# Optimization experiments

Hardware: AMD Instinct MI355X
Metric: run time of the kernel (lower is better)

Reference implementation:

```python
import jax, jax.numpy as jnp
import numpy as np

B, D, H, E = 4096, 256, 1024, 8


def setup_inputs() -> dict:
    key = jax.random.key(0)
    k_x, k_w1, k_b1, k_w2, k_b2, k_idx = jax.random.split(key, 6)
    return {
        "x": jax.random.normal(k_x, (B, D), dtype=jnp.float32),
        "W1": jax.random.normal(k_w1, (E, D, H), dtype=jnp.float32) * (1.0 / np.sqrt(D)),
        "b1": jax.random.normal(k_b1, (E, H), dtype=jnp.float32) * 0.01,
        "W2": jax.random.normal(k_w2, (E, H, D), dtype=jnp.float32) * (1.0 / np.sqrt(H)),
        "b2": jax.random.normal(k_b2, (E, D), dtype=jnp.float32) * 0.01,
        "expert_idx": jax.random.randint(k_idx, (B,), 0, E, dtype=jnp.int64)
        if jax.config.jax_enable_x64 else jax.random.randint(k_idx, (B,), 0, E, dtype=jnp.int32),
    }


def reference(x, W1, b1, W2, b2, expert_idx):
    # Each sample i is routed to expert expert_idx[i] (= video_id_to_index lookup),
    # runs the expert MLP on its batch-of-1 row, and results are concatenated.
    # Vectorized as: run all experts over the batch, combine with a one-hot mask.
    E_ = W1.shape[0]
    onehot = jax.nn.one_hot(expert_idx, E_, dtype=x.dtype)          # [B, E]
    h = jax.nn.relu(jnp.einsum("bd,edh->ebh", x, W1) + b1[:, None, :])  # [E, B, H]
    y = jnp.einsum("ebh,ehd->ebd", h, W2) + b2[:, None, :]              # [E, B, D]
    return jnp.einsum("be,ebd->bd", onehot, y)                           # [B, D]
```

## Files before the change

kernel.cpp:

```cpp
#include <hip/hip_runtime.h>


#define D_DIM 256
#define H_DIM 1024
#define E_NUM 8
#define B_TOK 4096
#define CAP   1024

typedef __attribute__((ext_vector_type(8))) short short8;
typedef __attribute__((ext_vector_type(4))) float f32x4;
typedef unsigned short u16;
typedef unsigned int u32;
typedef unsigned long long u64;

#define CNT_OFF    0
#define BUCKET_OFF 1024
#define XB_OFF     (BUCKET_OFF + E_NUM*B_TOK*4)
#define W1T_OFF    (XB_OFF  + (size_t)B_TOK*D_DIM*2)
#define W2T_OFF    (W1T_OFF + (size_t)E_NUM*H_DIM*D_DIM*2)
#define HW_OFF     (W2T_OFF + (size_t)E_NUM*D_DIM*H_DIM*2)

__device__ __forceinline__ u16 f2bf(float f) {
    u32 u = __builtin_bit_cast(u32, f);
    u = (u + 0x7fffu + ((u >> 16) & 1u)) >> 16;
    return (u16)u;
}

__device__ __forceinline__ void trans_load(const float* __restrict__ in, int C,
                                           int rt, int ct, int tt, u16* tile) {
    #pragma unroll
    for (int it = 0; it < 4; ++it) {
        int r = it * 16 + (tt >> 4);
        int c4 = (tt & 15) * 4;
        float4 v = *(const float4*)(in + (size_t)(rt * 64 + r) * C + ct * 64 + c4);
        u64 pk = (u64)f2bf(v.x) | ((u64)f2bf(v.y) << 16)
               | ((u64)f2bf(v.z) << 32) | ((u64)f2bf(v.w) << 48);
        *(u64*)&tile[r * 68 + c4] = pk;
    }
}

__device__ __forceinline__ uint4 trans_pack(const u16* tile, int oc, int r0) {
    u32 p0 = tile[(r0 + 0) * 68 + oc] | ((u32)tile[(r0 + 1) * 68 + oc] << 16);
    u32 p1 = tile[(r0 + 2) * 68 + oc] | ((u32)tile[(r0 + 3) * 68 + oc] << 16);
    u32 p2 = tile[(r0 + 4) * 68 + oc] | ((u32)tile[(r0 + 5) * 68 + oc] << 16);
    u32 p3 = tile[(r0 + 6) * 68 + oc] | ((u32)tile[(r0 + 7) * 68 + oc] << 16);
    return uint4{p0, p1, p2, p3};
}

__global__ __launch_bounds__(256) void prep_kernel(
    const float* __restrict__ x, const float* __restrict__ W1,
    const float* __restrict__ W2, const int* __restrict__ eidx,
    int* __restrict__ cnt, int* __restrict__ bucket,
    u16* __restrict__ xb, u16* __restrict__ w1t, u16* __restrict__ w2t)
{
    __shared__ u16 tile[64 * 68];
    const int b = blockIdx.x, tid = threadIdx.x;
    if (b < 8) {
        __shared__ int wsum[4];
        const int e = b;
        const int lane = tid & 63, wv = tid >> 6;
        int base = 0;
        #pragma unroll
        for (int c = 0; c < 16; ++c) {
            int t = c * 256 + tid;
            bool m = (eidx[t] == e);
            u64 bal = __ballot(m);
            int pfx = __popcll(bal & ((1ull << lane) - 1ull));
            if (lane == 0) wsum[wv] = __popcll(bal);
            __syncthreads();
            int wb = 0, total = 0;
            #pragma unroll
            for (int i = 0; i < 4; ++i) { if (i < wv) wb += wsum[i]; total += wsum[i]; }
            if (m) bucket[e * B_TOK + base + wb + pfx] = t;
            base += total;
            __syncthreads();
        }
        if (tid == 0) cnt[e] = base;
    } else if (b < 264) {
        int gb = b - 8;
        int row = gb * 16 + (tid >> 4);
        int sub = tid & 15;
        const float* src = x + (size_t)row * D_DIM + sub * 16;
        u16* dst = xb + (size_t)row * D_DIM + sub * 16;
        #pragma unroll
        for (int i = 0; i < 4; ++i) {
            float4 v = *(const float4*)(src + i * 4);
            u64 pk = (u64)f2bf(v.x) | ((u64)f2bf(v.y) << 16)
                   | ((u64)f2bf(v.z) << 32) | ((u64)f2bf(v.w) << 48);
            *(u64*)(dst + i * 4) = pk;
        }
    } else if (b < 776) {
        int bb = b - 264;
        int e = bb >> 6, tj = bb & 63;
        int rt = tj >> 4, ct = tj & 15;
        trans_load(W1 + (size_t)e * D_DIM * H_DIM, H_DIM, rt, ct, tid, tile);
        __syncthreads();
        u16* outp = w1t + (size_t)e * H_DIM * D_DIM;
        #pragma unroll
        for (int it = 0; it < 2; ++it) {
            int oc = it * 32 + (tid >> 3);
            int r0 = (tid & 7) * 8;
            *(uint4*)(outp + (size_t)(ct * 64 + oc) * D_DIM + rt * 64 + r0) =
                trans_pack(tile, oc, r0);
        }
    } else {
        int bb = b - 776;
        int e = bb >> 6, tj = bb & 63;
        int rt = tj >> 2, ct = tj & 3;
        trans_load(W2 + (size_t)e * H_DIM * D_DIM, D_DIM, rt, ct, tid, tile);
        __syncthreads();
        u16* outp = w2t + (size_t)e * D_DIM * H_DIM;
        #pragma unroll
        for (int it = 0; it < 2; ++it) {
            int oc = it * 32 + (tid >> 3);
            int r0 = (tid & 7) * 8;
            *(uint4*)(outp + (size_t)(ct * 64 + oc) * H_DIM + rt * 64 + r0) =
                trans_pack(tile, oc, r0);
        }
    }
}

__global__ __launch_bounds__(256, 2) void gemm1_kernel(
    const u16* __restrict__ xb, const u16* __restrict__ w1t,
    const float* __restrict__ b1, const int* __restrict__ cnt,
    const int* __restrict__ bucket, u16* __restrict__ hw)
{
    __shared__ u16 xs[64 * 264];
    __shared__ u16 w1s[64 * 264];
    __shared__ u16 hs[64 * 72];

    const int b = blockIdx.x;
    const int e = b >> 8, tile = (b >> 4) & 15, hch = b & 15;
    const int n = min(cnt[e], CAP);
    const int row0 = tile * 64;
    if (row0 >= n) return;

    const int tid = threadIdx.x;
    const int w = tid >> 6, L = tid & 63, l15 = L & 15, l4 = L >> 4;
    const int wr = (w >> 1) * 32, wc = (w & 1) * 32;

    {
        const int rr = tid >> 5, cc = (tid & 31) * 8;
        int tok[8];
        #pragma unroll
        for (int it = 0; it < 8; ++it) {
            int grow = row0 + it * 8 + rr;
            tok[it] = grow < n ? bucket[e * B_TOK + grow] : 0;
        }
        const u16* gw = w1t + ((size_t)e * H_DIM + hch * 64) * D_DIM;
        #pragma unroll
        for (int it = 0; it < 8; ++it) {
            int row = it * 8 + rr;
            *(short8*)&xs[row * 264 + cc]  = *(const short8*)&xb[(size_t)tok[it] * D_DIM + cc];
            *(short8*)&w1s[row * 264 + cc] = *(const short8*)&gw[(size_t)row * D_DIM + cc];
        }
    }
    __syncthreads();

    f32x4 acc[2][2];
    #pragma unroll
    for (int i = 0; i < 2; ++i)
        #pragma unroll
        for (int j = 0; j < 2; ++j) acc[i][j] = (f32x4){0.f, 0.f, 0.f, 0.f};

    #pragma unroll
    for (int k = 0; k < 8; ++k) {
        short8 a0 = *(const short8*)&xs[(wr + l15) * 264 + k * 32 + l4 * 8];
        short8 a1 = *(const short8*)&xs[(wr + 16 + l15) * 264 + k * 32 + l4 * 8];
        short8 b0 = *(const short8*)&w1s[(wc + l15) * 264 + k * 32 + l4 * 8];
        short8 b1v = *(const short8*)&w1s[(wc + 16 + l15) * 264 + k * 32 + l4 * 8];
        acc[0][0] = __builtin_amdgcn_mfma_f32_16x16x32_bf16(a0, b0, acc[0][0], 0, 0, 0);
        acc[0][1] = __builtin_amdgcn_mfma_f32_16x16x32_bf16(a0, b1v, acc[0][1], 0, 0, 0);
        acc[1][0] = __builtin_amdgcn_mfma_f32_16x16x32_bf16(a1, b0, acc[1][0], 0, 0, 0);
        acc[1][1] = __builtin_amdgcn_mfma_f32_16x16x32_bf16(a1, b1v, acc[1][1], 0, 0, 0);
    }

    #pragma unroll
    for (int mr = 0; mr < 2; ++mr)
        #pragma unroll
        for (int nc = 0; nc < 2; ++nc) {
            float bias = b1[e * H_DIM + hch * 64 + wc + nc * 16 + l15];
            #pragma unroll
            for (int j = 0; j < 4; ++j) {
                float v = fmaxf(acc[mr][nc][j] + bias, 0.f);
                hs[(wr + mr * 16 + l4 * 4 + j) * 72 + wc + nc * 16 + l15] = f2bf(v);
            }
        }
    __syncthreads();
    {
        u16* gh = hw + ((size_t)e * CAP + row0) * H_DIM + hch * 64;
        int rr8 = tid >> 3, off = (tid & 7) * 8;
        #pragma unroll
        for (int it = 0; it < 2; ++it) {
            int row = it * 32 + rr8;
            *(short8*)&gh[(size_t)row * H_DIM + off] = *(const short8*)&hs[row * 72 + off];
        }
    }
}

__global__ __launch_bounds__(256, 2) void gemm2_kernel(
    const u16* __restrict__ hw, const u16* __restrict__ w2t,
    const float* __restrict__ b2, const int* __restrict__ cnt,
    const int* __restrict__ bucket, float* __restrict__ out)
{
    __shared__ u16 as_[64 * 264];
    __shared__ u16 bs[64 * 264];

    int b = blockIdx.x;
    int e = b >> 6, tile = (b >> 2) & 15, nch = b & 3;
    int n = min(cnt[e], CAP);
    if (tile * 64 >= n) return;

    int tid = threadIdx.x;
    int w = tid >> 6, L = tid & 63, l15 = L & 15, l4 = L >> 4;
    int wr = (w >> 1) * 32, wc = (w & 1) * 32;

    f32x4 acc[2][2];
    #pragma unroll
    for (int i = 0; i < 2; ++i)
        #pragma unroll
        for (int j = 0; j < 2; ++j) acc[i][j] = (f32x4){0.f, 0.f, 0.f, 0.f};

    const u16* ga = hw + ((size_t)e * CAP + tile * 64) * H_DIM;
    const u16* gb = w2t + ((size_t)e * D_DIM + nch * 64) * H_DIM;

    for (int kc = 0; kc < 4; ++kc) {
        __syncthreads();
        int rr = tid >> 5, cc = (tid & 31) * 8;
        #pragma unroll
        for (int it = 0; it < 8; ++it) {
            int row = it * 8 + rr;
            *(short8*)&as_[row * 264 + cc] = *(const short8*)&ga[(size_t)row * H_DIM + kc * 256 + cc];
            *(short8*)&bs[row * 264 + cc]  = *(const short8*)&gb[(size_t)row * H_DIM + kc * 256 + cc];
        }
        __syncthreads();
        #pragma unroll
        for (int k = 0; k < 8; ++k) {
            short8 a0 = *(const short8*)&as_[(wr + l15) * 264 + k * 32 + l4 * 8];
            short8 a1 = *(const short8*)&as_[(wr + 16 + l15) * 264 + k * 32 + l4 * 8];
            short8 b0 = *(const short8*)&bs[(wc + l15) * 264 + k * 32 + l4 * 8];
            short8 b1v = *(const short8*)&bs[(wc + 16 + l15) * 264 + k * 32 + l4 * 8];
            acc[0][0] = __builtin_amdgcn_mfma_f32_16x16x32_bf16(a0, b0, acc[0][0], 0, 0, 0);
            acc[0][1] = __builtin_amdgcn_mfma_f32_16x16x32_bf16(a0, b1v, acc[0][1], 0, 0, 0);
            acc[1][0] = __builtin_amdgcn_mfma_f32_16x16x32_bf16(a1, b0, acc[1][0], 0, 0, 0);
            acc[1][1] = __builtin_amdgcn_mfma_f32_16x16x32_bf16(a1, b1v, acc[1][1], 0, 0, 0);
        }
    }

    #pragma unroll
    for (int mr = 0; mr < 2; ++mr)
        #pragma unroll
        for (int jj = 0; jj < 4; ++jj) {
            int m = wr + mr * 16 + l4 * 4 + jj;
            if (tile * 64 + m < n) {
                int token = bucket[e * B_TOK + tile * 64 + m];
                #pragma unroll
                for (int nc = 0; nc < 2; ++nc) {
                    int d = nch * 64 + wc + nc * 16 + l15;
                    out[(size_t)token * D_DIM + d] = acc[mr][nc][jj] + b2[e * D_DIM + d];
                }
            }
        }
}

extern "C" void kernel_launch(void* const* d_in, const int* in_sizes, int n_in,
                              void* d_out, int out_size, void* d_ws, size_t ws_size,
                              hipStream_t stream) {
    const float* x  = (const float*)d_in[0];
    const float* W1 = (const float*)d_in[1];
    const float* b1 = (const float*)d_in[2];
    const float* W2 = (const float*)d_in[3];
    const float* b2 = (const float*)d_in[4];
    const int* eidx = (const int*)d_in[5];
    float* out = (float*)d_out;

    char* ws = (char*)d_ws;
    int* cnt    = (int*)(ws + CNT_OFF);
    int* bucket = (int*)(ws + BUCKET_OFF);
    u16* xb     = (u16*)(ws + XB_OFF);
    u16* w1t    = (u16*)(ws + W1T_OFF);
    u16* w2t    = (u16*)(ws + W2T_OFF);
    u16* hw     = (u16*)(ws + HW_OFF);

    prep_kernel<<<1288, 256, 0, stream>>>(x, W1, W2, eidx, cnt, bucket, xb, w1t, w2t);
    gemm1_kernel<<<E_NUM * 16 * 16, 256, 0, stream>>>(xb, w1t, b1, cnt, bucket, hw);
    gemm2_kernel<<<E_NUM * 16 * 4, 256, 0, stream>>>(hw, w2t, b2, cnt, bucket, out);
}
```

Before: 41.67 us.

## Use single-wave blocks loading MFMA operands straight from global memory

Both expert GEMM kernels move from 256-thread blocks that stage 64x256 operand tiles in shared memory to 64-thread single-wave blocks. Each wave computes the whole 64x64 output tile with a 4x4 MFMA accumulator grid and reads its A and B fragments directly from global memory, relying on cache, with no LDS staging and no barriers. The aim is to drop shared-memory traffic and synchronisation and to raise occupancy. In exchange the wave issues uncoalesced strided global loads, has less latency hiding per block, and uses more registers.

After: 60.65 us. 45.5% more time.

```diff
diff --git a/kernel.cpp b/kernel.cpp
--- a/kernel.cpp
+++ b/kernel.cpp
@@ -120,144 +120,125 @@
     }
 }
 
-__global__ __launch_bounds__(256, 2) void gemm1_kernel(
+__global__ __launch_bounds__(64) void g1_kernel(
     const u16* __restrict__ xb, const u16* __restrict__ w1t,
     const float* __restrict__ b1, const int* __restrict__ cnt,
     const int* __restrict__ bucket, u16* __restrict__ hw)
 {
-    __shared__ u16 xs[64 * 264];
-    __shared__ u16 w1s[64 * 264];
-    __shared__ u16 hs[64 * 72];
+    __shared__ u16 hs[64 * 68];
 
     const int b = blockIdx.x;
-    const int e = b >> 8, tile = (b >> 4) & 15, hch = b & 15;
+    const int e = b >> 8, mt = (b >> 4) & 15, hch = b & 15;
     const int n = min(cnt[e], CAP);
-    const int row0 = tile * 64;
+    const int row0 = mt * 64;
     if (row0 >= n) return;
 
-    const int tid = threadIdx.x;
-    const int w = tid >> 6, L = tid & 63, l15 = L & 15, l4 = L >> 4;
-    const int wr = (w >> 1) * 32, wc = (w & 1) * 32;
-
-    {
-        const int rr = tid >> 5, cc = (tid & 31) * 8;
-        int tok[8];
-        #pragma unroll
-        for (int it = 0; it < 8; ++it) {
-            int grow = row0 + it * 8 + rr;
-            tok[it] = grow < n ? bucket[e * B_TOK + grow] : 0;
-        }
-        const u16* gw = w1t + ((size_t)e * H_DIM + hch * 64) * D_DIM;
-        #pragma unroll
-        for (int it = 0; it < 8; ++it) {
-            int row = it * 8 + rr;
-            *(short8*)&xs[row * 264 + cc]  = *(const short8*)&xb[(size_t)tok[it] * D_DIM + cc];
-            *(short8*)&w1s[row * 264 + cc] = *(const short8*)&gw[(size_t)row * D_DIM + cc];
-        }
-    }
-    __syncthreads();
-
-    f32x4 acc[2][2];
-    #pragma unroll
-    for (int i = 0; i < 2; ++i)
-        #pragma unroll
-        for (int j = 0; j < 2; ++j) acc[i][j] = (f32x4){0.f, 0.f, 0.f, 0.f};
+    const int L = threadIdx.x;
+    const int l15 = L & 15, l4 = L >> 4;
+
+    const u16* Ap[4];
+    #pragma unroll
+    for (int mr = 0; mr < 4; ++mr) {
+        int grow = row0 + mr * 16 + l15;
+        int tok = grow < n ? bucket[e * B_TOK + grow] : 0;
+        Ap[mr] = xb + (size_t)tok * D_DIM;
+    }
+    const u16* Bp = w1t + ((size_t)e * H_DIM + hch * 64) * D_DIM;
+
+    f32x4 acc[4][4];
+    #pragma unroll
+    for (int i = 0; i < 4; ++i)
+        #pragma unroll
+        for (int j = 0; j < 4; ++j) acc[i][j] = (f32x4){0.f, 0.f, 0.f, 0.f};
 
     #pragma unroll
     for (int k = 0; k < 8; ++k) {
-        short8 a0 = *(const short8*)&xs[(wr + l15) * 264 + k * 32 + l4 * 8];
-        short8 a1 = *(const short8*)&xs[(wr + 16 + l15) * 264 + k * 32 + l4 * 8];
-        short8 b0 = *(const short8*)&w1s[(wc + l15) * 264 + k * 32 + l4 * 8];
-        short8 b1v = *(const short8*)&w1s[(wc + 16 + l15) * 264 + k * 32 + l4 * 8];
-        acc[0][0] = __builtin_amdgcn_mfma_f32_16x16x32_bf16(a0, b0, acc[0][0], 0, 0, 0);
-        acc[0][1] = __builtin_amdgcn_mfma_f32_16x16x32_bf16(a0, b1v, acc[0][1], 0, 0, 0);
-        acc[1][0] = __builtin_amdgcn_mfma_f32_16x16x32_bf16(a1, b0, acc[1][0], 0, 0, 0);
-        acc[1][1] = __builtin_amdgcn_mfma_f32_16x16x32_bf16(a1, b1v, acc[1][1], 0, 0, 0);
-    }
-
-    #pragma unroll
-    for (int mr = 0; mr < 2; ++mr)
-        #pragma unroll
-        for (int nc = 0; nc < 2; ++nc) {
-            float bias = b1[e * H_DIM + hch * 64 + wc + nc * 16 + l15];
+        const int koff = k * 32 + l4 * 8;
+        short8 a0 = *(const short8*)(Ap[0] + koff);
+        short8 a1 = *(const short8*)(Ap[1] + koff);
+        short8 a2 = *(const short8*)(Ap[2] + koff);
+        short8 a3 = *(const short8*)(Ap[3] + koff);
+        #pragma unroll
+        for (int nc = 0; nc < 4; ++nc) {
+            short8 bf = *(const short8*)(Bp + (size_t)(nc * 16 + l15) * D_DIM + koff);
+            acc[0][nc] = __builtin_amdgcn_mfma_f32_16x16x32_bf16(a0, bf, acc[0][nc], 0, 0, 0);
+            acc[1][nc] = __builtin_amdgcn_mfma_f32_16x16x32_bf16(a1, bf, acc[1][nc], 0, 0, 0);
+            acc[2][nc] = __builtin_amdgcn_mfma_f32_16x16x32_bf16(a2, bf, acc[2][nc], 0, 0, 0);
+            acc[3][nc] = __builtin_amdgcn_mfma_f32_16x16x32_bf16(a3, bf, acc[3][nc], 0, 0, 0);
+        }
+    }
+
+    #pragma unroll
+    for (int nc = 0; nc < 4; ++nc) {
+        float bias = b1[e * H_DIM + hch * 64 + nc * 16 + l15];
+        #pragma unroll
+        for (int mr = 0; mr < 4; ++mr)
             #pragma unroll
             for (int j = 0; j < 4; ++j) {
                 float v = fmaxf(acc[mr][nc][j] + bias, 0.f);
-                hs[(wr + mr * 16 + l4 * 4 + j) * 72 + wc + nc * 16 + l15] = f2bf(v);
+                hs[(mr * 16 + l4 * 4 + j) * 68 + nc * 16 + l15] = f2bf(v);
             }
-        }
-    __syncthreads();
-    {
-        u16* gh = hw + ((size_t)e * CAP + row0) * H_DIM + hch * 64;
-        int rr8 = tid >> 3, off = (tid & 7) * 8;
-        #pragma unroll
-        for (int it = 0; it < 2; ++it) {
-            int row = it * 32 + rr8;
-            *(short8*)&gh[(size_t)row * H_DIM + off] = *(const short8*)&hs[row * 72 + off];
-        }
-    }
-}
-
-__global__ __launch_bounds__(256, 2) void gemm2_kernel(
+    }
+    #pragma unroll
+    for (int it = 0; it < 8; ++it) {
+        int row = it * 8 + (L >> 3);
+        int i = L & 7;
+        short8 v = *(const short8*)&hs[row * 68 + i * 8];
+        *(short8*)(hw + ((size_t)e * CAP + row0 + row) * H_DIM + hch * 64 + i * 8) = v;
+    }
+}
+
+__global__ __launch_bounds__(64) void g2_kernel(
     const u16* __restrict__ hw, const u16* __restrict__ w2t,
     const float* __restrict__ b2, const int* __restrict__ cnt,
     const int* __restrict__ bucket, float* __restrict__ out)
 {
-    __shared__ u16 as_[64 * 264];
-    __shared__ u16 bs[64 * 264];
-
-    int b = blockIdx.x;
-    int e = b >> 6, tile = (b >> 2) & 15, nch = b & 3;
-    int n = min(cnt[e], CAP);
-    if (tile * 64 >= n) return;
-
-    int tid = threadIdx.x;
-    int w = tid >> 6, L = tid & 63, l15 = L & 15, l4 = L >> 4;
-    int wr = (w >> 1) * 32, wc = (w & 1) * 32;
-
-    f32x4 acc[2][2];
-    #pragma unroll
-    for (int i = 0; i < 2; ++i)
-        #pragma unroll
-        for (int j = 0; j < 2; ++j) acc[i][j] = (f32x4){0.f, 0.f, 0.f, 0.f};
-
-    const u16* ga = hw + ((size_t)e * CAP + tile * 64) * H_DIM;
-    const u16* gb = w2t + ((size_t)e * D_DIM + nch * 64) * H_DIM;
-
-    for (int kc = 0; kc < 4; ++kc) {
-        __syncthreads();
-        int rr = tid >> 5, cc = (tid & 31) * 8;
-        #pragma unroll
-        for (int it = 0; it < 8; ++it) {
-            int row = it * 8 + rr;
-            *(short8*)&as_[row * 264 + cc] = *(const short8*)&ga[(size_t)row * H_DIM + kc * 256 + cc];
-            *(short8*)&bs[row * 264 + cc]  = *(const short8*)&gb[(size_t)row * H_DIM + kc * 256 + cc];
-        }
-        __syncthreads();
-        #pragma unroll
-        for (int k = 0; k < 8; ++k) {
-            short8 a0 = *(const short8*)&as_[(wr + l15) * 264 + k * 32 + l4 * 8];
-            short8 a1 = *(const short8*)&as_[(wr + 16 + l15) * 264 + k * 32 + l4 * 8];
-            short8 b0 = *(const short8*)&bs[(wc + l15) * 264 + k * 32 + l4 * 8];
-            short8 b1v = *(const short8*)&bs[(wc + 16 + l15) * 264 + k * 32 + l4 * 8];
-            acc[0][0] = __builtin_amdgcn_mfma_f32_16x16x32_bf16(a0, b0, acc[0][0], 0, 0, 0);
-            acc[0][1] = __builtin_amdgcn_mfma_f32_16x16x32_bf16(a0, b1v, acc[0][1], 0, 0, 0);
-            acc[1][0] = __builtin_amdgcn_mfma_f32_16x16x32_bf16(a1, b0, acc[1][0], 0, 0, 0);
-            acc[1][1] = __builtin_amdgcn_mfma_f32_16x16x32_bf16(a1, b1v, acc[1][1], 0, 0, 0);
-        }
-    }
-
-    #pragma unroll
-    for (int mr = 0; mr < 2; ++mr)
-        #pragma unroll
-        for (int jj = 0; jj < 4; ++jj) {
-            int m = wr + mr * 16 + l4 * 4 + jj;
-            if (tile * 64 + m < n) {
-                int token = bucket[e * B_TOK + tile * 64 + m];
+    const int b = blockIdx.x;
+    const int e = b >> 6, mt = (b >> 2) & 15, nch = b & 3;
+    const int n = min(cnt[e], CAP);
+    const int row0 = mt * 64;
+    if (row0 >= n) return;
+
+    const int L = threadIdx.x;
+    const int l15 = L & 15, l4 = L >> 4;
+
+    const u16* Ab = hw + ((size_t)e * CAP + row0) * H_DIM;
+    const u16* Bb = w2t + ((size_t)e * D_DIM + nch * 64) * H_DIM;
+
+    f32x4 acc[4][4];
+    #pragma unroll
+    for (int i = 0; i < 4; ++i)
+        #pragma unroll
+        for (int j = 0; j < 4; ++j) acc[i][j] = (f32x4){0.f, 0.f, 0.f, 0.f};
+
+    #pragma unroll 2
+    for (int k = 0; k < 32; ++k) {
+        const int koff = k * 32 + l4 * 8;
+        short8 a0 = *(const short8*)(Ab + (size_t)(l15)      * H_DIM + koff);
+        short8 a1 = *(const short8*)(Ab + (size_t)(16 + l15) * H_DIM + koff);
+        short8 a2 = *(const short8*)(Ab + (size_t)(32 + l15) * H_DIM + koff);
+        short8 a3 = *(const short8*)(Ab + (size_t)(48 + l15) * H_DIM + koff);
+        #pragma unroll
+        for (int nc = 0; nc < 4; ++nc) {
+            short8 bf = *(const short8*)(Bb + (size_t)(nc * 16 + l15) * H_DIM + koff);
+            acc[0][nc] = __builtin_amdgcn_mfma_f32_16x16x32_bf16(a0, bf, acc[0][nc], 0, 0, 0);
+            acc[1][nc] = __builtin_amdgcn_mfma_f32_16x16x32_bf16(a1, bf, acc[1][nc], 0, 0, 0);
+            acc[2][nc] = __builtin_amdgcn_mfma_f32_16x16x32_bf16(a2, bf, acc[2][nc], 0, 0, 0);
+            acc[3][nc] = __builtin_amdgcn_mfma_f32_16x16x32_bf16(a3, bf, acc[3][nc], 0, 0, 0);
+        }
+    }
+
+    #pragma unroll
+    for (int mr = 0; mr < 4; ++mr)
+        #pragma unroll
+        for (int j = 0; j < 4; ++j) {
+            int m = mr * 16 + l4 * 4 + j;
+            if (row0 + m < n) {
+                int token = bucket[e * B_TOK + row0 + m];
                 #pragma unroll
-                for (int nc = 0; nc < 2; ++nc) {
-                    int d = nch * 64 + wc + nc * 16 + l15;
-                    out[(size_t)token * D_DIM + d] = acc[mr][nc][jj] + b2[e * D_DIM + d];
+                for (int nc = 0; nc < 4; ++nc) {
+                    int d = nch * 64 + nc * 16 + l15;
+                    out[(size_t)token * D_DIM + d] = acc[mr][nc][j] + b2[e * D_DIM + d];
                 }
             }
         }
@@ -283,6 +264,6 @@
     u16* hw     = (u16*)(ws + HW_OFF);
 
     prep_kernel<<<1288, 256, 0, stream>>>(x, W1, W2, eidx, cnt, bucket, xb, w1t, w2t);
-    gemm1_kernel<<<E_NUM * 16 * 16, 256, 0, stream>>>(xb, w1t, b1, cnt, bucket, hw);
-    gemm2_kernel<<<E_NUM * 16 * 4, 256, 0, stream>>>(hw, w2t, b2, cnt, bucket, out);
-}
+    g1_kernel<<<E_NUM * 16 * 16, 64, 0, stream>>>(xb, w1t, b1, cnt, bucket, hw);
+    g2_kernel<<<E_NUM * 16 * 4, 64, 0, stream>>>(hw, w2t, b2, cnt, bucket, out);
+}
```
